# Kernel tuning notes

Hardware: AMD Instinct MI355X
Metric: run time of the kernel (lower is better)

The kernel has to match this reference:

```python
import jax, jax.numpy as jnp
import numpy as np

B, N, D, E, FF_MULT = 2, 1024, 1024, 8, 4
H = D * FF_MULT


def setup_inputs() -> dict:
    key = jax.random.key(0)
    k = jax.random.split(key, 6)
    tokens = jax.random.normal(k[0], (B, N, D), dtype=jnp.float32)
    # uniform(0,1): strictly positive -> every expert processes every token
    dispatch_weights = jax.random.uniform(k[1], (B, N, E), dtype=jnp.float32)
    combine_weights = jax.random.uniform(k[2], (B, N, E), dtype=jnp.float32)
    # per-expert SwiGLU params, stacked on leading expert axis.
    # stored pre-transposed: y = x @ W  (torch Linear weight is [out,in])
    xavier_dh = np.sqrt(2.0 / (D + H))
    Wg = jax.random.normal(k[3], (E, D, H), dtype=jnp.float32) * xavier_dh
    Wv = jax.random.normal(k[4], (E, D, H), dtype=jnp.float32) * xavier_dh
    Wo = jax.random.normal(k[5], (E, H, D), dtype=jnp.float32) * (0.02 * xavier_dh)
    scale = jnp.full((E,), 1.0 / E, dtype=jnp.float32)  # output_scale init 1/E
    return {"tokens": tokens, "dispatch_weights": dispatch_weights,
            "combine_weights": combine_weights, "Wg": Wg, "Wv": Wv,
            "Wo": Wo, "scale": scale}


def reference(tokens, dispatch_weights, combine_weights, Wg, Wv, Wo, scale):
    b, n, d = tokens.shape
    x = tokens.reshape(b * n, d)                      # (T, D)
    disp = dispatch_weights.reshape(b * n, E)         # (T, E)
    comb = combine_weights.reshape(b * n, E)          # (T, E)
    # SwiGLU FFN for all experts at once (dense grouped GEMM)
    gate = jax.nn.gelu(jnp.einsum('td,edh->teh', x, Wg), approximate=False)
    value = jnp.einsum('td,edh->teh', x, Wv)
    expert_out = jnp.einsum('teh,ehd->ted', gate * value, Wo)  # (T, E, D)
    expert_out = expert_out * scale[None, :, None]
    # combine: weight by combine_weights where dispatched (dispatch > 0)
    w = jnp.where(disp > 0, comb, 0.0)                # (T, E)
    output = jnp.einsum('ted,te->td', expert_out, w)
    return output.reshape(b, n, d)
```

## Files before the change

kernel.cpp:

```cpp
#include <hip/hip_runtime.h>
#include <math.h>

#define T_TOK 2048
#define DDIM 1024
#define HDIM 4096
#define NEXP 8
#define NPRIME 8192
#define KTOT (NEXP * HDIM)
#define NSPLIT 8

typedef unsigned short u16;
typedef __attribute__((ext_vector_type(4))) float f32x4;
typedef __attribute__((ext_vector_type(8))) __bf16 bf16x8;
typedef __attribute__((ext_vector_type(8))) unsigned short u16x8;
typedef __attribute__((ext_vector_type(4))) unsigned short u16x4;

__device__ __forceinline__ u16 f2bf(float f) {
  unsigned int u = __builtin_bit_cast(unsigned int, f);
  u += 0x7fffu + ((u >> 16) & 1u);
  return (u16)(u >> 16);
}

__device__ __forceinline__ void stage16(const u16* g, u16* l) {
  __builtin_amdgcn_global_load_lds((__attribute__((address_space(1))) void*)g,
                                   (__attribute__((address_space(3))) void*)l,
                                   16, 0, 0);
}

__global__ void cvt_x_kernel(const float* __restrict__ x, u16* __restrict__ xb) {
  int i = (blockIdx.x * 256 + threadIdx.x) * 8;
  float4 a = *(const float4*)(x + i);
  float4 b = *(const float4*)(x + i + 4);
  u16x8 o;
  o[0] = f2bf(a.x); o[1] = f2bf(a.y); o[2] = f2bf(a.z); o[3] = f2bf(a.w);
  o[4] = f2bf(b.x); o[5] = f2bf(b.y); o[6] = f2bf(b.z); o[7] = f2bf(b.w);
  *(u16x8*)(xb + i) = o;
}

__global__ void transpose_all_kernel(const float* __restrict__ Wg,
                                     const float* __restrict__ Wv,
                                     const float* __restrict__ Wo,
                                     u16* __restrict__ wgvT, u16* __restrict__ woT2) {
  __shared__ float lds[64][65];
  const int bid = blockIdx.x;
  const int e = bid / 3072;
  const int r = bid % 3072;
  const int which = r >> 10;
  const int tt = r & 1023;
  const float* src; int R, C;
  if (which == 2) { src = Wo + (size_t)e * HDIM * DDIM; R = HDIM; C = DDIM; }
  else            { src = (which ? Wv : Wg) + (size_t)e * DDIM * HDIM; R = DDIM; C = HDIM; }
  const int nrt = R >> 6;
  const int r0 = (tt % nrt) << 6, c0 = (tt / nrt) << 6;
  const int tid = threadIdx.x;
#pragma unroll
  for (int i = 0; i < 4; ++i) {
    int f4 = tid + 256 * i;
    int row = f4 >> 4, c4 = (f4 & 15) << 2;
    float4 v = *(const float4*)(src + (size_t)(r0 + row) * C + c0 + c4);
    lds[row][c4] = v.x; lds[row][c4 + 1] = v.y; lds[row][c4 + 2] = v.z; lds[row][c4 + 3] = v.w;
  }
  __syncthreads();
#pragma unroll
  for (int i = 0; i < 4; ++i) {
    int f4 = tid + 256 * i;
    int cc = f4 >> 4, r4 = (f4 & 15) << 2;
    u16x4 o;
    o[0] = f2bf(lds[r4][cc]);     o[1] = f2bf(lds[r4 + 1][cc]);
    o[2] = f2bf(lds[r4 + 2][cc]); o[3] = f2bf(lds[r4 + 3][cc]);
    u16* dst;
    if (which == 2) {
      dst = woT2 + (size_t)(c0 + cc) * KTOT + e * HDIM + r0 + r4;
    } else {
      int h = c0 + cc;
      int rowp = ((h >> 4) << 5) + which * 16 + (h & 15);
      dst = wgvT + (size_t)e * NPRIME * DDIM + (size_t)rowp * DDIM + r0 + r4;
    }
    *(u16x4*)dst = o;
  }
}


template<int KS>
__device__ __forceinline__ void gemm_loop(const u16* Ab, const u16* Bb,
                                          int Am0, int Bn0, int kbase, int NT,
                                          u16* lds, int tid, f32x4 (&acc)[8][4]) {
  const int lane = tid & 63;
  const int wave = tid >> 6;
  const int wm = wave >> 2, wn = wave & 3;
  const int l15 = lane & 15, lkq = lane >> 4;

  const int sl = tid & 7, rw = tid >> 3;
  const int slx = (sl ^ (rw & 7)) << 3;
  const int rb = (rw & 31) + ((rw >> 5) << 6);
  const u16* pA = Ab + (size_t)(Am0 + rw) * KS + kbase + slx;
  const u16* pB = Bb + (size_t)(Bn0 + rb) * KS + kbase + slx;
  const int dA = rw * 64 + sl * 8;
  const int dB = 16384 + rb * 64 + sl * 8;

  auto slot = [&](int t) -> u16* { return lds + (t & 1) * 32768; };
  auto SA0 = [&](int t) { u16* sp = slot(t); const int k = t << 6;
    stage16(pA + k, sp + dA);
    stage16(pA + (size_t)128 * KS + k, sp + dA + 8192); };
  auto SA1 = [&](int t) { u16* sp = slot(t); const int k = t << 6;
    stage16(pA + (size_t)64 * KS + k, sp + dA + 4096);
    stage16(pA + (size_t)192 * KS + k, sp + dA + 12288); };
  auto SB0 = [&](int t) { u16* sp = slot(t); const int k = t << 6;
    stage16(pB + k, sp + dB);
    stage16(pB + (size_t)128 * KS + k, sp + dB + 8192); };
  auto SB1 = [&](int t) { u16* sp = slot(t); const int k = t << 6;
    stage16(pB + (size_t)32 * KS + k, sp + dB + 2048);
    stage16(pB + (size_t)160 * KS + k, sp + dB + 10240); };

  const int swz0 = (lkq ^ (l15 & 7)) << 3;
  const int swz1 = ((4 | lkq) ^ (l15 & 7)) << 3;
  const int arow = (wm * 128 + l15) * 64;
  const int brow = 16384 + (wn * 64 + l15) * 64;
  const int a0 = arow + swz0, a1 = arow + swz1;
  const int b0 = brow + swz0, b1 = brow + swz1;

  SA0(0); SB0(0); SB1(0); SA1(0);
  SA0(1); SB0(1); SB1(1);
  asm volatile("s_waitcnt vmcnt(10)" ::: "memory");
  __builtin_amdgcn_s_barrier();

#pragma unroll 1
  for (int t = 0; t < NT; ++t) {
    const u16* s = slot(t);
    const int tp1 = (t + 1 < NT) ? t + 1 : NT - 1;
    const int tp2 = (t + 2 < NT) ? t + 2 : NT - 1;
    bf16x8 af[4][2], bfr[4][2];

#pragma unroll
    for (int mf = 0; mf < 4; ++mf) {
      af[mf][0] = *(const bf16x8*)(s + a0 + mf * 1024);
      af[mf][1] = *(const bf16x8*)(s + a1 + mf * 1024);
    }
#pragma unroll
    for (int nf = 0; nf < 2; ++nf) {
      bfr[nf][0] = *(const bf16x8*)(s + b0 + nf * 1024);
      bfr[nf][1] = *(const bf16x8*)(s + b1 + nf * 1024);
    }
    SA1(tp1);
    asm volatile("s_waitcnt vmcnt(10)" ::: "memory");
    __builtin_amdgcn_s_barrier();
    asm volatile("s_waitcnt lgkmcnt(0)" ::: "memory");
    __builtin_amdgcn_sched_barrier(0);
    __builtin_amdgcn_s_setprio(1);
#pragma unroll
    for (int ks = 0; ks < 2; ++ks)
#pragma unroll
      for (int mf = 0; mf < 4; ++mf)
#pragma unroll
        for (int nf = 0; nf < 2; ++nf)
          acc[mf][nf] = __builtin_amdgcn_mfma_f32_16x16x32_bf16(af[mf][ks], bfr[nf][ks], acc[mf][nf], 0, 0, 0);
    __builtin_amdgcn_s_setprio(0);
    __builtin_amdgcn_s_barrier();

#pragma unroll
    for (int nf = 2; nf < 4; ++nf) {
      bfr[nf][0] = *(const bf16x8*)(s + b0 + nf * 1024);
      bfr[nf][1] = *(const bf16x8*)(s + b1 + nf * 1024);
    }
    SA0(tp2);
    asm volatile("s_waitcnt vmcnt(10)" ::: "memory");
    __builtin_amdgcn_s_barrier();
    asm volatile("s_waitcnt lgkmcnt(0)" ::: "memory");
    __builtin_amdgcn_sched_barrier(0);
    __builtin_amdgcn_s_setprio(1);
#pragma unroll
    for (int ks = 0; ks < 2; ++ks)
#pragma unroll
      for (int mf = 0; mf < 4; ++mf)
#pragma unroll
        for (int nf = 2; nf < 4; ++nf)
          acc[mf][nf] = __builtin_amdgcn_mfma_f32_16x16x32_bf16(af[mf][ks], bfr[nf][ks], acc[mf][nf], 0, 0, 0);
    __builtin_amdgcn_s_setprio(0);
    __builtin_amdgcn_s_barrier();

#pragma unroll
    for (int mf = 0; mf < 4; ++mf) {
      af[mf][0] = *(const bf16x8*)(s + a0 + 4096 + mf * 1024);
      af[mf][1] = *(const bf16x8*)(s + a1 + 4096 + mf * 1024);
    }
    SB0(tp2);
    __builtin_amdgcn_s_barrier();
    asm volatile("s_waitcnt lgkmcnt(0)" ::: "memory");
    __builtin_amdgcn_sched_barrier(0);
    __builtin_amdgcn_s_setprio(1);
#pragma unroll
    for (int ks = 0; ks < 2; ++ks)
#pragma unroll
      for (int mf = 0; mf < 4; ++mf)
#pragma unroll
        for (int nf = 0; nf < 2; ++nf)
          acc[4 + mf][nf] = __builtin_amdgcn_mfma_f32_16x16x32_bf16(af[mf][ks], bfr[nf][ks], acc[4 + mf][nf], 0, 0, 0);
    __builtin_amdgcn_s_setprio(0);
    __builtin_amdgcn_s_barrier();

    SB1(tp2);
    asm volatile("s_waitcnt vmcnt(10)" ::: "memory");
    __builtin_amdgcn_s_barrier();
    __builtin_amdgcn_s_setprio(1);
#pragma unroll
    for (int ks = 0; ks < 2; ++ks)
#pragma unroll
      for (int mf = 0; mf < 4; ++mf)
#pragma unroll
        for (int nf = 2; nf < 4; ++nf)
          acc[4 + mf][nf] = __builtin_amdgcn_mfma_f32_16x16x32_bf16(af[mf][ks], bfr[nf][ks], acc[4 + mf][nf], 0, 0, 0);
    __builtin_amdgcn_s_setprio(0);
    __builtin_amdgcn_s_barrier();
  }
}

__global__ void __launch_bounds__(512, 2)
gemm_gv_kernel(const u16* __restrict__ xb, const u16* __restrict__ wgvT,
               const float* __restrict__ disp, const float* __restrict__ comb,
               const float* __restrict__ scale, u16* __restrict__ h) {
  __shared__ u16 lds[65536];

  const int bid = blockIdx.x;
  const int wg = (bid & 7) * 256 + (bid >> 3);
  const int e  = wg >> 8;
  const int rr = wg & 255;
  const int nt = rr >> 3;
  const int mt = rr & 7;

  const int tid = threadIdx.x;
  const int lane = tid & 63;
  const int wave = tid >> 6;
  const int wm = wave >> 2, wn = wave & 3;
  const int l15 = lane & 15, lkq = lane >> 4;

  const u16* Bb = wgvT + (size_t)e * NPRIME * DDIM;
  const int Am0 = mt * 256;
  const int Bn0 = nt * 256;

  f32x4 acc[8][4] = {};
  gemm_loop<DDIM>(xb, Bb, Am0, Bn0, 0, DDIM / 64, lds, tid, acc);

  const float s_e = scale[e];
  const int hbase = nt * 128 + wn * 32;
#pragma unroll
  for (int a = 0; a < 8; ++a) {
#pragma unroll
    for (int r = 0; r < 4; ++r) {
      const int t = Am0 + wm * 128 + a * 16 + lkq * 4 + r;
      const float dv = disp[t * NEXP + e];
      const float cv = comb[t * NEXP + e];
      const float s = (dv > 0.0f) ? cv * s_e : 0.0f;
#pragma unroll
      for (int jj = 0; jj < 2; ++jj) {
        const float g = acc[a][2 * jj][r];
        const float v = acc[a][2 * jj + 1][r];
        const float ge = 0.5f * g * (1.0f + erff(g * 0.70710678f));
        h[(size_t)t * KTOT + e * HDIM + hbase + jj * 16 + l15] = f2bf(ge * v * s);
      }
    }
  }
}

__global__ void __launch_bounds__(512, 2)
gemm_out_kernel(const u16* __restrict__ hb, const u16* __restrict__ woT2,
                float* __restrict__ P) {
  __shared__ u16 lds[65536];

  const int bid = blockIdx.x;
  const int wg = (bid & 7) * 32 + (bid >> 3);
  const int kz = wg >> 5;
  const int rr = wg & 31;
  const int nt = rr >> 3;
  const int mt = rr & 7;

  const int tid = threadIdx.x;
  const int lane = tid & 63;
  const int wave = tid >> 6;
  const int wm = wave >> 2, wn = wave & 3;
  const int l15 = lane & 15, lkq = lane >> 4;

  const int Am0 = mt * 256;
  const int Bn0 = nt * 256;
  const int kbase = kz * (KTOT / NSPLIT);

  f32x4 acc[8][4] = {};
  gemm_loop<KTOT>(hb, woT2, Am0, Bn0, kbase, (KTOT / NSPLIT) / 64, lds, tid, acc);

  float* Pp = P + (size_t)kz * (T_TOK * DDIM);
#pragma unroll
  for (int a = 0; a < 8; ++a) {
#pragma unroll
    for (int r = 0; r < 4; ++r) {
      const int t = Am0 + wm * 128 + a * 16 + lkq * 4 + r;
#pragma unroll
      for (int nf = 0; nf < 4; ++nf)
        Pp[(size_t)t * DDIM + Bn0 + wn * 64 + nf * 16 + l15] = acc[a][nf][r];
    }
  }
}

__global__ void reduce_out_kernel(const float* __restrict__ P, float* __restrict__ out) {
  int i = blockIdx.x * 256 + threadIdx.x;
  float4 a = ((const float4*)P)[i];
#pragma unroll
  for (int s = 1; s < NSPLIT; ++s) {
    float4 b = ((const float4*)P)[i + s * (T_TOK * DDIM / 4)];
    a.x += b.x; a.y += b.y; a.z += b.z; a.w += b.w;
  }
  ((float4*)out)[i] = a;
}

extern "C" void kernel_launch(void* const* d_in, const int* in_sizes, int n_in,
                              void* d_out, int out_size, void* d_ws, size_t ws_size,
                              hipStream_t stream) {
  const float* tokens = (const float*)d_in[0];
  const float* disp   = (const float*)d_in[1];
  const float* comb   = (const float*)d_in[2];
  const float* Wg     = (const float*)d_in[3];
  const float* Wv     = (const float*)d_in[4];
  const float* Wo     = (const float*)d_in[5];
  const float* scale  = (const float*)d_in[6];
  float* out = (float*)d_out;

  char* ws = (char*)d_ws;
  const size_t MB = 1024 * 1024;
  u16* xb    = (u16*)(ws);
  u16* wgvT  = (u16*)(ws + 4   * MB);
  u16* woT2  = (u16*)(ws + 132 * MB);
  u16* hbuf  = (u16*)(ws + 196 * MB);
  float* P   = (float*)(ws + 324 * MB);

  cvt_x_kernel<<<1024, 256, 0, stream>>>(tokens, xb);
  transpose_all_kernel<<<24576, 256, 0, stream>>>(Wg, Wv, Wo, wgvT, woT2);
  gemm_gv_kernel<<<2048, 512, 0, stream>>>(xb, wgvT, disp, comb, scale, hbuf);
  gemm_out_kernel<<<256, 512, 0, stream>>>(hbuf, woT2, P);
  reduce_out_kernel<<<2048, 256, 0, stream>>>(P, out);
}
```

Baseline: 549.0 us.

## Load gate/value GEMM A-operand directly into registers, stage only B in LDS

Rewrites the gate/value GEMM kernel so each wave loads its token-row (A) fragments straight from global memory into registers instead of staging them through LDS. Only the weight tile (B) is double-buffered in LDS, which halves the shared-memory footprint and cuts LDS traffic. The main loop is restructured to interleave the A-fragment global loads with MFMA groups. In exchange it raises register pressure and relies on global/L2 latency being hidden behind the MFMA work.

```diff
diff --git a/kernel.cpp b/kernel.cpp
--- a/kernel.cpp
+++ b/kernel.cpp
@@ -80,6 +80,151 @@
   }
 }
 
+__global__ void __launch_bounds__(512, 2)
+gemm_gv_kernel(const u16* __restrict__ xb, const u16* __restrict__ wgvT,
+               const float* __restrict__ disp, const float* __restrict__ comb,
+               const float* __restrict__ scale, u16* __restrict__ h) {
+  __shared__ u16 lds[32768];
+
+  const int bid = blockIdx.x;
+  const int wg = (bid & 7) * 256 + (bid >> 3);
+  const int e  = wg >> 8;
+  const int rr = wg & 255;
+  const int nt = rr >> 3;
+  const int mt = rr & 7;
+
+  const int tid = threadIdx.x;
+  const int lane = tid & 63;
+  const int wave = tid >> 6;
+  const int wm = wave >> 2, wn = wave & 3;
+  const int l15 = lane & 15, lkq = lane >> 4;
+
+  const u16* Bb = wgvT + (size_t)e * NPRIME * DDIM;
+  const int Am0 = mt * 256;
+  const int Bn0 = nt * 256;
+
+  const u16* pB[4]; int dB[4];
+#pragma unroll
+  for (int i = 0; i < 4; ++i) {
+    int c = tid + 512 * i, row = c >> 3, sl2 = c & 7;
+    pB[i] = Bb + (size_t)(Bn0 + row) * DDIM + ((sl2 ^ (row & 7)) << 3);
+    dB[i] = row * 64 + sl2 * 8;
+  }
+  const int b0 = (wn * 64 + l15) * 64 + ((lkq ^ (l15 & 7)) << 3);
+  const int b1 = (wn * 64 + l15) * 64 + (((4 | lkq) ^ (l15 & 7)) << 3);
+  const u16* pAl = xb + (size_t)(Am0 + wm * 128 + l15) * DDIM + lkq * 8;
+
+  f32x4 acc[8][4] = {};
+  bf16x8 af[8][2], bfr[4][2];
+  const int NT = DDIM / 64;
+
+#pragma unroll
+  for (int i = 0; i < 4; ++i) stage16(pB[i], lds + dB[i]);
+#pragma unroll
+  for (int mf = 0; mf < 8; ++mf) {
+    af[mf][0] = *(const bf16x8*)(pAl + mf * 16 * DDIM);
+    af[mf][1] = *(const bf16x8*)(pAl + mf * 16 * DDIM + 32);
+  }
+  asm volatile("s_waitcnt vmcnt(16)" ::: "memory");
+  __builtin_amdgcn_s_barrier();
+
+#pragma unroll 1
+  for (int t = 0; t < NT; ++t) {
+    const u16* sB = lds + (t & 1) * 16384;
+    u16* sBn = lds + ((t & 1) ^ 1) * 16384;
+    const int tp1 = (t + 1 < NT) ? t + 1 : NT - 1;
+    const int kn = tp1 << 6;
+
+#pragma unroll
+    for (int nf = 0; nf < 2; ++nf) {
+      bfr[nf][0] = *(const bf16x8*)(sB + b0 + nf * 1024);
+      bfr[nf][1] = *(const bf16x8*)(sB + b1 + nf * 1024);
+    }
+#pragma unroll
+    for (int i = 0; i < 4; ++i) stage16(pB[i] + kn, sBn + dB[i]);
+    __builtin_amdgcn_sched_barrier(0);
+    __builtin_amdgcn_s_setprio(1);
+#pragma unroll
+    for (int ks = 0; ks < 2; ++ks)
+#pragma unroll
+      for (int mf = 0; mf < 4; ++mf)
+#pragma unroll
+        for (int nf = 0; nf < 2; ++nf)
+          acc[mf][nf] = __builtin_amdgcn_mfma_f32_16x16x32_bf16(af[mf][ks], bfr[nf][ks], acc[mf][nf], 0, 0, 0);
+    __builtin_amdgcn_s_setprio(0);
+
+#pragma unroll
+    for (int nf = 2; nf < 4; ++nf) {
+      bfr[nf][0] = *(const bf16x8*)(sB + b0 + nf * 1024);
+      bfr[nf][1] = *(const bf16x8*)(sB + b1 + nf * 1024);
+    }
+    __builtin_amdgcn_s_setprio(1);
+#pragma unroll
+    for (int ks = 0; ks < 2; ++ks)
+#pragma unroll
+      for (int mf = 0; mf < 4; ++mf)
+#pragma unroll
+        for (int nf = 2; nf < 4; ++nf)
+          acc[mf][nf] = __builtin_amdgcn_mfma_f32_16x16x32_bf16(af[mf][ks], bfr[nf][ks], acc[mf][nf], 0, 0, 0);
+    __builtin_amdgcn_s_setprio(0);
+    __builtin_amdgcn_sched_barrier(0);
+#pragma unroll
+    for (int mf = 0; mf < 4; ++mf) {
+      af[mf][0] = *(const bf16x8*)(pAl + mf * 16 * DDIM + kn);
+      af[mf][1] = *(const bf16x8*)(pAl + mf * 16 * DDIM + kn + 32);
+    }
+    __builtin_amdgcn_sched_barrier(0);
+
+    __builtin_amdgcn_s_setprio(1);
+#pragma unroll
+    for (int ks = 0; ks < 2; ++ks)
+#pragma unroll
+      for (int mf = 0; mf < 4; ++mf)
+#pragma unroll
+        for (int nf = 0; nf < 2; ++nf)
+          acc[4 + mf][nf] = __builtin_amdgcn_mfma_f32_16x16x32_bf16(af[4 + mf][ks], bfr[nf][ks], acc[4 + mf][nf], 0, 0, 0);
+    __builtin_amdgcn_s_setprio(0);
+
+    __builtin_amdgcn_s_setprio(1);
+#pragma unroll
+    for (int ks = 0; ks < 2; ++ks)
+#pragma unroll
+      for (int mf = 0; mf < 4; ++mf)
+#pragma unroll
+        for (int nf = 2; nf < 4; ++nf)
+          acc[4 + mf][nf] = __builtin_amdgcn_mfma_f32_16x16x32_bf16(af[4 + mf][ks], bfr[nf][ks], acc[4 + mf][nf], 0, 0, 0);
+    __builtin_amdgcn_s_setprio(0);
+    __builtin_amdgcn_sched_barrier(0);
+#pragma unroll
+    for (int mf = 4; mf < 8; ++mf) {
+      af[mf][0] = *(const bf16x8*)(pAl + mf * 16 * DDIM + kn);
+      af[mf][1] = *(const bf16x8*)(pAl + mf * 16 * DDIM + kn + 32);
+    }
+    __builtin_amdgcn_sched_barrier(0);
+    asm volatile("s_waitcnt vmcnt(16)" ::: "memory");
+    __builtin_amdgcn_s_barrier();
+  }
+
+  const float s_e = scale[e];
+  const int hbase = nt * 128 + wn * 32;
+#pragma unroll
+  for (int a = 0; a < 8; ++a) {
+#pragma unroll
+    for (int r = 0; r < 4; ++r) {
+      const int t = Am0 + wm * 128 + a * 16 + lkq * 4 + r;
+      const float dv = disp[t * NEXP + e];
+      const float cv = comb[t * NEXP + e];
+      const float s = (dv > 0.0f) ? cv * s_e : 0.0f;
+#pragma unroll
+      for (int jj = 0; jj < 2; ++jj) {
+        const float g = acc[a][2 * jj][r];
+        const float v = acc[a][2 * jj + 1][r];
+        const float ge = 0.5f * g * (1.0f + erff(g * 0.70710678f));
+        h[(size_t)t * KTOT + e * HDIM + hbase + jj * 16 + l15] = f2bf(ge * v * s);
+      }
+    }
+  }
+}
 
 template<int KS>
 __device__ __forceinline__ void gemm_loop(const u16* Ab, const u16* Bb,
@@ -215,53 +360,6 @@
 }
 
 __global__ void __launch_bounds__(512, 2)
-gemm_gv_kernel(const u16* __restrict__ xb, const u16* __restrict__ wgvT,
-               const float* __restrict__ disp, const float* __restrict__ comb,
-               const float* __restrict__ scale, u16* __restrict__ h) {
-  __shared__ u16 lds[65536];
-
-  const int bid = blockIdx.x;
-  const int wg = (bid & 7) * 256 + (bid >> 3);
-  const int e  = wg >> 8;
-  const int rr = wg & 255;
-  const int nt = rr >> 3;
-  const int mt = rr & 7;
-
-  const int tid = threadIdx.x;
-  const int lane = tid & 63;
-  const int wave = tid >> 6;
-  const int wm = wave >> 2, wn = wave & 3;
-  const int l15 = lane & 15, lkq = lane >> 4;
-
-  const u16* Bb = wgvT + (size_t)e * NPRIME * DDIM;
-  const int Am0 = mt * 256;
-  const int Bn0 = nt * 256;
-
-  f32x4 acc[8][4] = {};
-  gemm_loop<DDIM>(xb, Bb, Am0, Bn0, 0, DDIM / 64, lds, tid, acc);
-
-  const float s_e = scale[e];
-  const int hbase = nt * 128 + wn * 32;
-#pragma unroll
-  for (int a = 0; a < 8; ++a) {
-#pragma unroll
-    for (int r = 0; r < 4; ++r) {
-      const int t = Am0 + wm * 128 + a * 16 + lkq * 4 + r;
-      const float dv = disp[t * NEXP + e];
-      const float cv = comb[t * NEXP + e];
-      const float s = (dv > 0.0f) ? cv * s_e : 0.0f;
-#pragma unroll
-      for (int jj = 0; jj < 2; ++jj) {
-        const float g = acc[a][2 * jj][r];
-        const float v = acc[a][2 * jj + 1][r];
-        const float ge = 0.5f * g * (1.0f + erff(g * 0.70710678f));
-        h[(size_t)t * KTOT + e * HDIM + hbase + jj * 16 + l15] = f2bf(ge * v * s);
-      }
-    }
-  }
-}
-
-__global__ void __launch_bounds__(512, 2)
 gemm_out_kernel(const u16* __restrict__ hb, const u16* __restrict__ woT2,
                 float* __restrict__ P) {
   __shared__ u16 lds[65536];
```

Result: slower. 876.1 us (+59.6%).

## Simplify GEMM main loop to two-phase double buffer with one-tile prefetch

Applied to the files above, without the earlier changes.

Replaces the four-phase GEMM inner loop with a two-phase loop. The old loop interleaved A/B sub-tile staging two tiles ahead using partial vmcnt waits and many barriers. The new loop loads all A/B fragments for each k-half, issues the staging of the next tile, runs 32 MFMAs per half, then drains all global loads with vmcnt(0) and a single barrier per iteration. This cuts barriers and lgkm waits, but gives up prefetch depth. The full drain each iteration risks exposing global-load latency.

```diff
diff --git a/kernel.cpp b/kernel.cpp
--- a/kernel.cpp
+++ b/kernel.cpp
@@ -98,17 +98,17 @@
   const int dA = rw * 64 + sl * 8;
   const int dB = 16384 + rb * 64 + sl * 8;
 
-  auto slot = [&](int t) -> u16* { return lds + (t & 1) * 32768; };
-  auto SA0 = [&](int t) { u16* sp = slot(t); const int k = t << 6;
+  auto slotp = [&](int t) -> u16* { return lds + (t & 1) * 32768; };
+  auto SA0 = [&](int t) { u16* sp = slotp(t); const int k = t << 6;
     stage16(pA + k, sp + dA);
     stage16(pA + (size_t)128 * KS + k, sp + dA + 8192); };
-  auto SA1 = [&](int t) { u16* sp = slot(t); const int k = t << 6;
+  auto SA1 = [&](int t) { u16* sp = slotp(t); const int k = t << 6;
     stage16(pA + (size_t)64 * KS + k, sp + dA + 4096);
     stage16(pA + (size_t)192 * KS + k, sp + dA + 12288); };
-  auto SB0 = [&](int t) { u16* sp = slot(t); const int k = t << 6;
+  auto SB0 = [&](int t) { u16* sp = slotp(t); const int k = t << 6;
     stage16(pB + k, sp + dB);
     stage16(pB + (size_t)128 * KS + k, sp + dB + 8192); };
-  auto SB1 = [&](int t) { u16* sp = slot(t); const int k = t << 6;
+  auto SB1 = [&](int t) { u16* sp = slotp(t); const int k = t << 6;
     stage16(pB + (size_t)32 * KS + k, sp + dB + 2048);
     stage16(pB + (size_t)160 * KS + k, sp + dB + 10240); };
 
@@ -120,96 +120,42 @@
   const int b0 = brow + swz0, b1 = brow + swz1;
 
   SA0(0); SB0(0); SB1(0); SA1(0);
-  SA0(1); SB0(1); SB1(1);
-  asm volatile("s_waitcnt vmcnt(10)" ::: "memory");
+  asm volatile("s_waitcnt vmcnt(0)" ::: "memory");
   __builtin_amdgcn_s_barrier();
 
 #pragma unroll 1
   for (int t = 0; t < NT; ++t) {
-    const u16* s = slot(t);
+    const u16* s = slotp(t);
     const int tp1 = (t + 1 < NT) ? t + 1 : NT - 1;
-    const int tp2 = (t + 2 < NT) ? t + 2 : NT - 1;
-    bf16x8 af[4][2], bfr[4][2];
-
-#pragma unroll
-    for (int mf = 0; mf < 4; ++mf) {
-      af[mf][0] = *(const bf16x8*)(s + a0 + mf * 1024);
-      af[mf][1] = *(const bf16x8*)(s + a1 + mf * 1024);
-    }
-#pragma unroll
-    for (int nf = 0; nf < 2; ++nf) {
-      bfr[nf][0] = *(const bf16x8*)(s + b0 + nf * 1024);
-      bfr[nf][1] = *(const bf16x8*)(s + b1 + nf * 1024);
-    }
-    SA1(tp1);
-    asm volatile("s_waitcnt vmcnt(10)" ::: "memory");
-    __builtin_amdgcn_s_barrier();
-    asm volatile("s_waitcnt lgkmcnt(0)" ::: "memory");
-    __builtin_amdgcn_sched_barrier(0);
+    bf16x8 af[8], bfr[4];
+
+#pragma unroll
+    for (int mf = 0; mf < 8; ++mf) af[mf] = *(const bf16x8*)(s + a0 + mf * 1024);
+#pragma unroll
+    for (int nf = 0; nf < 4; ++nf) bfr[nf] = *(const bf16x8*)(s + b0 + nf * 1024);
+    SA0(tp1); SB0(tp1);
     __builtin_amdgcn_s_setprio(1);
 #pragma unroll
-    for (int ks = 0; ks < 2; ++ks)
-#pragma unroll
-      for (int mf = 0; mf < 4; ++mf)
-#pragma unroll
-        for (int nf = 0; nf < 2; ++nf)
-          acc[mf][nf] = __builtin_amdgcn_mfma_f32_16x16x32_bf16(af[mf][ks], bfr[nf][ks], acc[mf][nf], 0, 0, 0);
+    for (int mf = 0; mf < 8; ++mf)
+#pragma unroll
+      for (int nf = 0; nf < 4; ++nf)
+        acc[mf][nf] = __builtin_amdgcn_mfma_f32_16x16x32_bf16(af[mf], bfr[nf], acc[mf][nf], 0, 0, 0);
     __builtin_amdgcn_s_setprio(0);
-    __builtin_amdgcn_s_barrier();
-
-#pragma unroll
-    for (int nf = 2; nf < 4; ++nf) {
-      bfr[nf][0] = *(const bf16x8*)(s + b0 + nf * 1024);
-      bfr[nf][1] = *(const bf16x8*)(s + b1 + nf * 1024);
-    }
-    SA0(tp2);
-    asm volatile("s_waitcnt vmcnt(10)" ::: "memory");
-    __builtin_amdgcn_s_barrier();
-    asm volatile("s_waitcnt lgkmcnt(0)" ::: "memory");
-    __builtin_amdgcn_sched_barrier(0);
+
+#pragma unroll
+    for (int mf = 0; mf < 8; ++mf) af[mf] = *(const bf16x8*)(s + a1 + mf * 1024);
+#pragma unroll
+    for (int nf = 0; nf < 4; ++nf) bfr[nf] = *(const bf16x8*)(s + b1 + nf * 1024);
+    SB1(tp1); SA1(tp1);
     __builtin_amdgcn_s_setprio(1);
 #pragma unroll
-    for (int ks = 0; ks < 2; ++ks)
-#pragma unroll
-      for (int mf = 0; mf < 4; ++mf)
-#pragma unroll
-        for (int nf = 2; nf < 4; ++nf)
-          acc[mf][nf] = __builtin_amdgcn_mfma_f32_16x16x32_bf16(af[mf][ks], bfr[nf][ks], acc[mf][nf], 0, 0, 0);
+    for (int mf = 0; mf < 8; ++mf)
+#pragma unroll
+      for (int nf = 0; nf < 4; ++nf)
+        acc[mf][nf] = __builtin_amdgcn_mfma_f32_16x16x32_bf16(af[mf], bfr[nf], acc[mf][nf], 0, 0, 0);
     __builtin_amdgcn_s_setprio(0);
-    __builtin_amdgcn_s_barrier();
-
-#pragma unroll
-    for (int mf = 0; mf < 4; ++mf) {
-      af[mf][0] = *(const bf16x8*)(s + a0 + 4096 + mf * 1024);
-      af[mf][1] = *(const bf16x8*)(s + a1 + 4096 + mf * 1024);
-    }
-    SB0(tp2);
-    __builtin_amdgcn_s_barrier();
-    asm volatile("s_waitcnt lgkmcnt(0)" ::: "memory");
-    __builtin_amdgcn_sched_barrier(0);
-    __builtin_amdgcn_s_setprio(1);
-#pragma unroll
-    for (int ks = 0; ks < 2; ++ks)
-#pragma unroll
-      for (int mf = 0; mf < 4; ++mf)
-#pragma unroll
-        for (int nf = 0; nf < 2; ++nf)
-          acc[4 + mf][nf] = __builtin_amdgcn_mfma_f32_16x16x32_bf16(af[mf][ks], bfr[nf][ks], acc[4 + mf][nf], 0, 0, 0);
-    __builtin_amdgcn_s_setprio(0);
-    __builtin_amdgcn_s_barrier();
-
-    SB1(tp2);
-    asm volatile("s_waitcnt vmcnt(10)" ::: "memory");
-    __builtin_amdgcn_s_barrier();
-    __builtin_amdgcn_s_setprio(1);
-#pragma unroll
-    for (int ks = 0; ks < 2; ++ks)
-#pragma unroll
-      for (int mf = 0; mf < 4; ++mf)
-#pragma unroll
-        for (int nf = 2; nf < 4; ++nf)
-          acc[4 + mf][nf] = __builtin_amdgcn_mfma_f32_16x16x32_bf16(af[mf][ks], bfr[nf][ks], acc[4 + mf][nf], 0, 0, 0);
-    __builtin_amdgcn_s_setprio(0);
+
+    asm volatile("s_waitcnt vmcnt(0)" ::: "memory");
     __builtin_amdgcn_s_barrier();
   }
 }
```

Measured after the change: 566.4 us. 1.03x slower.

## Use 256x128-tile 4-wave GEMM for gate/value and tanh-approx GELU

Applied to the files above, without the earlier changes.

Replaces the gate/value GEMM's 512-thread 256x256 tile with a 256-thread 256x128 tile. The new main loop keeps the A tile in a single buffer, double-buffers the B tile, and overlaps global-to-LDS loads with MFMAs. The launch doubles to 4096 blocks. The exact erf GELU is swapped for a tanh approximation built from exp2 and rcp, which lowers epilogue cost but changes numerics slightly. The smaller tile lowers arithmetic intensity per block, in exchange for more blocks and a simpler pipeline.

```diff
diff --git a/kernel.cpp b/kernel.cpp
--- a/kernel.cpp
+++ b/kernel.cpp
@@ -19,6 +19,14 @@
   unsigned int u = __builtin_bit_cast(unsigned int, f);
   u += 0x7fffu + ((u >> 16) & 1u);
   return (u16)(u >> 16);
+}
+
+__device__ __forceinline__ float fast_gelu(float g) {
+  float g2 = g * g;
+  float y  = g * (0.7978845608f + 0.0356774081f * g2);
+  float e  = __builtin_amdgcn_exp2f(2.8853901817f * y);
+  float t  = 1.0f - 2.0f * __builtin_amdgcn_rcpf(1.0f + e);
+  return 0.5f * g * (1.0f + t);
 }
 
 __device__ __forceinline__ void stage16(const u16* g, u16* l) {
@@ -80,11 +88,133 @@
   }
 }
 
-
 template<int KS>
-__device__ __forceinline__ void gemm_loop(const u16* Ab, const u16* Bb,
-                                          int Am0, int Bn0, int kbase, int NT,
-                                          u16* lds, int tid, f32x4 (&acc)[8][4]) {
+__device__ __forceinline__ void gemm_loop4(const u16* Ab, const u16* Bb,
+                                           int Am0, int Bn0, int kbase, int NT,
+                                           u16* lds, int tid, f32x4 (&acc)[8][4]) {
+  const int lane = tid & 63;
+  const int wave = tid >> 6;
+  const int wm = wave >> 1, wn = wave & 1;
+  const int l15 = lane & 15, lkq = lane >> 4;
+
+  const int sl = tid & 7, r0 = tid >> 3;
+  const int slx = (sl ^ (r0 & 7)) << 3;
+  const u16* pA = Ab + (size_t)(Am0 + r0) * KS + kbase + slx;
+  const u16* pB = Bb + (size_t)(Bn0 + r0) * KS + kbase + slx;
+  const int dA0 = r0 * 64 + sl * 8;
+  const int dB0 = r0 * 64 + sl * 8;
+
+  const int swz0 = (lkq ^ (l15 & 7)) << 3;
+  const int swz1 = ((4 | lkq) ^ (l15 & 7)) << 3;
+  const int arow = (wm * 128 + l15) * 64;
+  const int brow = (wn * 64 + l15) * 64;
+  const int a0 = arow + swz0, a1 = arow + swz1;
+  const int b0 = brow + swz0, b1 = brow + swz1;
+
+#pragma unroll
+  for (int i = 0; i < 8; ++i) stage16(pA + (size_t)(i * 32) * KS, lds + dA0 + i * 2048);
+#pragma unroll
+  for (int i = 0; i < 4; ++i) stage16(pB + (size_t)(i * 32) * KS, lds + 16384 + dB0 + i * 2048);
+  asm volatile("s_waitcnt vmcnt(0)" ::: "memory");
+  __builtin_amdgcn_s_barrier();
+
+#pragma unroll 1
+  for (int t = 0; t < NT; ++t) {
+    const int bs = 16384 + ((t & 1) << 13);
+    const int bn = 16384 + (((t + 1) & 1) << 13);
+    const int tp1 = (t + 1 < NT) ? t + 1 : NT - 1;
+    const size_t kn = (size_t)(tp1 << 6);
+    bf16x8 af[8][2], bfr[4];
+
+#pragma unroll
+    for (int mf = 0; mf < 8; ++mf) {
+      af[mf][0] = *(const bf16x8*)(lds + a0 + mf * 1024);
+      af[mf][1] = *(const bf16x8*)(lds + a1 + mf * 1024);
+    }
+#pragma unroll
+    for (int nf = 0; nf < 4; ++nf) bfr[nf] = *(const bf16x8*)(lds + bs + b0 + nf * 1024);
+    asm volatile("s_waitcnt lgkmcnt(0)" ::: "memory");
+    __builtin_amdgcn_s_barrier();
+
+#pragma unroll
+    for (int i = 0; i < 8; ++i) stage16(pA + (size_t)(i * 32) * KS + kn, lds + dA0 + i * 2048);
+#pragma unroll
+    for (int i = 0; i < 4; ++i) stage16(pB + (size_t)(i * 32) * KS + kn, lds + bn + dB0 + i * 2048);
+    __builtin_amdgcn_sched_barrier(0);
+
+    __builtin_amdgcn_s_setprio(1);
+#pragma unroll
+    for (int mf = 0; mf < 8; ++mf)
+#pragma unroll
+      for (int nf = 0; nf < 4; ++nf)
+        acc[mf][nf] = __builtin_amdgcn_mfma_f32_16x16x32_bf16(af[mf][0], bfr[nf], acc[mf][nf], 0, 0, 0);
+    __builtin_amdgcn_s_setprio(0);
+
+#pragma unroll
+    for (int nf = 0; nf < 4; ++nf) bfr[nf] = *(const bf16x8*)(lds + bs + b1 + nf * 1024);
+    __builtin_amdgcn_s_setprio(1);
+#pragma unroll
+    for (int mf = 0; mf < 8; ++mf)
+#pragma unroll
+      for (int nf = 0; nf < 4; ++nf)
+        acc[mf][nf] = __builtin_amdgcn_mfma_f32_16x16x32_bf16(af[mf][1], bfr[nf], acc[mf][nf], 0, 0, 0);
+    __builtin_amdgcn_s_setprio(0);
+
+    asm volatile("s_waitcnt vmcnt(0)" ::: "memory");
+    __builtin_amdgcn_s_barrier();
+  }
+}
+
+__global__ void __launch_bounds__(256, 2)
+gemm_gv_kernel(const u16* __restrict__ xb, const u16* __restrict__ wgvT,
+               const float* __restrict__ disp, const float* __restrict__ comb,
+               const float* __restrict__ scale, u16* __restrict__ h) {
+  __shared__ u16 lds[32768];
+
+  const int bid = blockIdx.x;
+  const int wg = (bid & 7) * 512 + (bid >> 3);
+  const int e  = wg >> 9;
+  const int rr = wg & 511;
+  const int nt = rr >> 3;
+  const int mt = rr & 7;
+
+  const int tid = threadIdx.x;
+  const int lane = tid & 63;
+  const int wave = tid >> 6;
+  const int wm = wave >> 1, wn = wave & 1;
+  const int l15 = lane & 15, lkq = lane >> 4;
+
+  const u16* Bb = wgvT + (size_t)e * NPRIME * DDIM;
+  const int Am0 = mt * 256;
+  const int Bn0 = nt * 128;
+
+  f32x4 acc[8][4] = {};
+  gemm_loop4<DDIM>(xb, Bb, Am0, Bn0, 0, DDIM / 64, lds, tid, acc);
+
+  const float s_e = scale[e];
+  const int hbase = nt * 64 + wn * 32;
+#pragma unroll
+  for (int a = 0; a < 8; ++a) {
+#pragma unroll
+    for (int r = 0; r < 4; ++r) {
+      const int t = Am0 + wm * 128 + a * 16 + lkq * 4 + r;
+      const float dv = disp[t * NEXP + e];
+      const float cv = comb[t * NEXP + e];
+      const float s = (dv > 0.0f) ? cv * s_e : 0.0f;
+#pragma unroll
+      for (int jj = 0; jj < 2; ++jj) {
+        const float g = acc[a][2 * jj][r];
+        const float v = acc[a][2 * jj + 1][r];
+        h[(size_t)t * KTOT + e * HDIM + hbase + jj * 16 + l15] = f2bf(fast_gelu(g) * v * s);
+      }
+    }
+  }
+}
+
+template<int KS>
+__device__ __forceinline__ void gemm_loop8(const u16* Ab, const u16* Bb,
+                                           int Am0, int Bn0, int kbase, int NT,
+                                           u16* lds, int tid, f32x4 (&acc)[8][4]) {
   const int lane = tid & 63;
   const int wave = tid >> 6;
   const int wm = wave >> 2, wn = wave & 3;
@@ -215,53 +345,6 @@
 }
 
 __global__ void __launch_bounds__(512, 2)
-gemm_gv_kernel(const u16* __restrict__ xb, const u16* __restrict__ wgvT,
-               const float* __restrict__ disp, const float* __restrict__ comb,
-               const float* __restrict__ scale, u16* __restrict__ h) {
-  __shared__ u16 lds[65536];
-
-  const int bid = blockIdx.x;
-  const int wg = (bid & 7) * 256 + (bid >> 3);
-  const int e  = wg >> 8;
-  const int rr = wg & 255;
-  const int nt = rr >> 3;
-  const int mt = rr & 7;
-
-  const int tid = threadIdx.x;
-  const int lane = tid & 63;
-  const int wave = tid >> 6;
-  const int wm = wave >> 2, wn = wave & 3;
-  const int l15 = lane & 15, lkq = lane >> 4;
-
-  const u16* Bb = wgvT + (size_t)e * NPRIME * DDIM;
-  const int Am0 = mt * 256;
-  const int Bn0 = nt * 256;
-
-  f32x4 acc[8][4] = {};
-  gemm_loop<DDIM>(xb, Bb, Am0, Bn0, 0, DDIM / 64, lds, tid, acc);
-
-  const float s_e = scale[e];
-  const int hbase = nt * 128 + wn * 32;
-#pragma unroll
-  for (int a = 0; a < 8; ++a) {
-#pragma unroll
-    for (int r = 0; r < 4; ++r) {
-      const int t = Am0 + wm * 128 + a * 16 + lkq * 4 + r;
-      const float dv = disp[t * NEXP + e];
-      const float cv = comb[t * NEXP + e];
-      const float s = (dv > 0.0f) ? cv * s_e : 0.0f;
-#pragma unroll
-      for (int jj = 0; jj < 2; ++jj) {
-        const float g = acc[a][2 * jj][r];
-        const float v = acc[a][2 * jj + 1][r];
-        const float ge = 0.5f * g * (1.0f + erff(g * 0.70710678f));
-        h[(size_t)t * KTOT + e * HDIM + hbase + jj * 16 + l15] = f2bf(ge * v * s);
-      }
-    }
-  }
-}
-
-__global__ void __launch_bounds__(512, 2)
 gemm_out_kernel(const u16* __restrict__ hb, const u16* __restrict__ woT2,
                 float* __restrict__ P) {
   __shared__ u16 lds[65536];
@@ -284,7 +367,7 @@
   const int kbase = kz * (KTOT / NSPLIT);
 
   f32x4 acc[8][4] = {};
-  gemm_loop<KTOT>(hb, woT2, Am0, Bn0, kbase, (KTOT / NSPLIT) / 64, lds, tid, acc);
+  gemm_loop8<KTOT>(hb, woT2, Am0, Bn0, kbase, (KTOT / NSPLIT) / 64, lds, tid, acc);
 
   float* Pp = P + (size_t)kz * (T_TOK * DDIM);
 #pragma unroll
@@ -332,7 +415,7 @@
 
   cvt_x_kernel<<<1024, 256, 0, stream>>>(tokens, xb);
   transpose_all_kernel<<<24576, 256, 0, stream>>>(Wg, Wv, Wo, wgvT, woT2);
-  gemm_gv_kernel<<<2048, 512, 0, stream>>>(xb, wgvT, disp, comb, scale, hbuf);
+  gemm_gv_kernel<<<4096, 256, 0, stream>>>(xb, wgvT, disp, comb, scale, hbuf);
   gemm_out_kernel<<<256, 512, 0, stream>>>(hbuf, woT2, P);
   reduce_out_kernel<<<2048, 256, 0, stream>>>(P, out);
 }
```

New measurement: 513.0 us. -6.6%, faster.
